# Optimization experiments

Measured on AMD Instinct MI355X. Metric: run time of the kernel, lower is better.

Reference implementation:

```python
import jax, jax.numpy as jnp
import numpy as np

D = H = W = 128
C = 16
VOXEL_SIZE = 0.05  # origin = 0, grid spans [0, 6.4]^3 in world coords
N_POINTS = 2_000_000


def setup_inputs() -> dict:
    key = jax.random.key(0)
    k1, k2 = jax.random.split(key)
    # world-space query points uniformly inside the grid bounds
    points = jax.random.uniform(k1, (N_POINTS, 3), dtype=jnp.float32) * (D * VOXEL_SIZE)
    values = jax.random.normal(k2, (D, H, W, C), dtype=jnp.float32)
    return {"points": points, "values": values}


def reference(points, values):
    # world -> grid coords (origin = 0)
    gc = points / VOXEL_SIZE  # [N, 3]
    x, y, z = gc[:, 0], gc[:, 1], gc[:, 2]

    x0 = jnp.clip(jnp.floor(x).astype(jnp.int32), 0, D - 1)
    y0 = jnp.clip(jnp.floor(y).astype(jnp.int32), 0, H - 1)
    z0 = jnp.clip(jnp.floor(z).astype(jnp.int32), 0, W - 1)
    x1 = jnp.clip(x0 + 1, 0, D - 1)
    y1 = jnp.clip(y0 + 1, 0, H - 1)
    z1 = jnp.clip(z0 + 1, 0, W - 1)

    # fractional offsets (computed against the clipped floor index, as in source)
    xd = (x - x0.astype(x.dtype))[:, None]
    yd = (y - y0.astype(y.dtype))[:, None]
    zd = (z - z0.astype(z.dtype))[:, None]

    # flatten grid for efficient single-axis gather
    flat = values.reshape(D * H * W, C)

    def gather(xi, yi, zi):
        lin = (xi * H + yi) * W + zi  # [N]
        return jnp.take(flat, lin, axis=0)  # [N, C]

    c000 = gather(x0, y0, z0)
    c001 = gather(x0, y0, z1)
    c010 = gather(x0, y1, z0)
    c011 = gather(x0, y1, z1)
    c100 = gather(x1, y0, z0)
    c101 = gather(x1, y0, z1)
    c110 = gather(x1, y1, z0)
    c111 = gather(x1, y1, z1)

    c00 = c000 * (1 - xd) + c100 * xd
    c01 = c001 * (1 - xd) + c101 * xd
    c10 = c010 * (1 - xd) + c110 * xd
    c11 = c011 * (1 - xd) + c111 * xd
    c0 = c00 * (1 - yd) + c10 * yd
    c1 = c01 * (1 - yd) + c11 * yd
    return c0 * (1 - zd) + c1 * zd  # [N, C]
```

## Files before the change

kernel.cpp:

```cpp
#include <hip/hip_runtime.h>


#define DD 128
#define HH 128
#define WW 128

__device__ __forceinline__ float4 lerp4(float4 a, float4 b, float t) {
    return make_float4(fmaf(b.x - a.x, t, a.x),
                       fmaf(b.y - a.y, t, a.y),
                       fmaf(b.z - a.z, t, a.z),
                       fmaf(b.w - a.w, t, a.w));
}

__global__ __launch_bounds__(256) void trilerp_kernel(
    const float* __restrict__ points,
    const float4* __restrict__ values,
    float4* __restrict__ out,
    int n_points)
{
    int t = blockIdx.x * blockDim.x + threadIdx.x;
    int p = t >> 2;
    int c4 = t & 3;
    if (p >= n_points) return;

    float x = points[p * 3 + 0] * 20.0f;
    float y = points[p * 3 + 1] * 20.0f;
    float z = points[p * 3 + 2] * 20.0f;

    float fx = floorf(x), fy = floorf(y), fz = floorf(z);
    int x0 = min(max((int)fx, 0), DD - 1);
    int y0 = min(max((int)fy, 0), HH - 1);
    int z0 = min(max((int)fz, 0), WW - 1);
    int x1 = min(x0 + 1, DD - 1);
    int y1 = min(y0 + 1, HH - 1);
    int z1 = min(z0 + 1, WW - 1);

    float xd = x - (float)x0;
    float yd = y - (float)y0;
    float zd = z - (float)z0;

    #define VIDX(xi, yi, zi) (((((xi) << 7) + (yi)) << 7) + (zi)) * 4 + c4

    float4 c000 = values[VIDX(x0, y0, z0)];
    float4 c001 = values[VIDX(x0, y0, z1)];
    float4 c010 = values[VIDX(x0, y1, z0)];
    float4 c011 = values[VIDX(x0, y1, z1)];
    float4 c100 = values[VIDX(x1, y0, z0)];
    float4 c101 = values[VIDX(x1, y0, z1)];
    float4 c110 = values[VIDX(x1, y1, z0)];
    float4 c111 = values[VIDX(x1, y1, z1)];
    #undef VIDX

    float4 c00 = lerp4(c000, c100, xd);
    float4 c01 = lerp4(c001, c101, xd);
    float4 c10 = lerp4(c010, c110, xd);
    float4 c11 = lerp4(c011, c111, xd);

    float4 c0 = lerp4(c00, c10, yd);
    float4 c1 = lerp4(c01, c11, yd);

    out[t] = lerp4(c0, c1, zd);
}

extern "C" void kernel_launch(void* const* d_in, const int* in_sizes, int n_in,
                              void* d_out, int out_size, void* d_ws, size_t ws_size,
                              hipStream_t stream) {
    const float* points = (const float*)d_in[0];
    const float4* values = (const float4*)d_in[1];
    float4* out = (float4*)d_out;

    int n_points = in_sizes[0] / 3;
    int total_threads = n_points * 4;
    int blocks = (total_threads + 255) / 256;

    trilerp_kernel<<<blocks, 256, 0, stream>>>(points, values, out, n_points);
}
```

Before: 414.7 us.

## Bucket-sort query points spatially before trilinear gather for cache locality

Adds a counting sort of points into 4x4x4-voxel buckets: a histogram pass, a single-block scan and an atomic scatter into a workspace buffer of (x,y,z,index). The interpolation kernel then walks the sorted points, so neighbouring threads gather nearby voxels, and writes results back by original index. This targets the random-access cost of the 128 MB value grid at the price of extra passes over the points, global atomics, scattered output writes and several more launches. A direct path is kept for when the workspace is too small.

```diff
diff --git a/kernel.cpp b/kernel.cpp
--- a/kernel.cpp
+++ b/kernel.cpp
@@ -1,9 +1,60 @@
 #include <hip/hip_runtime.h>
+#include <hip/hip_runtime_api.h>
 
 
 #define DD 128
 #define HH 128
 #define WW 128
+#define NBUCKET 32768
+
+__device__ __forceinline__ int bucket_of(float px, float py, float pz) {
+    int x0 = min(max((int)floorf(px * 20.0f), 0), DD - 1);
+    int y0 = min(max((int)floorf(py * 20.0f), 0), HH - 1);
+    int z0 = min(max((int)floorf(pz * 20.0f), 0), WW - 1);
+    return (((x0 >> 2) << 5) + (y0 >> 2)) * 32 + (z0 >> 2);
+}
+
+__global__ __launch_bounds__(256) void hist_kernel(
+    const float* __restrict__ points, unsigned int* __restrict__ hist, int n)
+{
+    int p = blockIdx.x * blockDim.x + threadIdx.x;
+    if (p >= n) return;
+    float px = points[3 * p + 0], py = points[3 * p + 1], pz = points[3 * p + 2];
+    atomicAdd(&hist[bucket_of(px, py, pz)], 1u);
+}
+
+__global__ __launch_bounds__(1024) void scan_kernel(
+    const unsigned int* __restrict__ hist, unsigned int* __restrict__ offsets)
+{
+    __shared__ unsigned int partial[1024];
+    int t = threadIdx.x;
+    unsigned int vals[32];
+    unsigned int sum = 0;
+    #pragma unroll
+    for (int i = 0; i < 32; ++i) { vals[i] = hist[t * 32 + i]; sum += vals[i]; }
+    partial[t] = sum;
+    __syncthreads();
+    for (int off = 1; off < 1024; off <<= 1) {
+        unsigned int v = (t >= off) ? partial[t - off] : 0u;
+        __syncthreads();
+        partial[t] += v;
+        __syncthreads();
+    }
+    unsigned int run = (t == 0) ? 0u : partial[t - 1];
+    #pragma unroll
+    for (int i = 0; i < 32; ++i) { offsets[t * 32 + i] = run; run += vals[i]; }
+}
+
+__global__ __launch_bounds__(256) void scatter_kernel(
+    const float* __restrict__ points, unsigned int* __restrict__ offsets,
+    float4* __restrict__ sorted, int n)
+{
+    int p = blockIdx.x * blockDim.x + threadIdx.x;
+    if (p >= n) return;
+    float px = points[3 * p + 0], py = points[3 * p + 1], pz = points[3 * p + 2];
+    unsigned int pos = atomicAdd(&offsets[bucket_of(px, py, pz)], 1u);
+    sorted[pos] = make_float4(px, py, pz, __int_as_float(p));
+}
 
 __device__ __forceinline__ float4 lerp4(float4 a, float4 b, float t) {
     return make_float4(fmaf(b.x - a.x, t, a.x),
@@ -12,8 +63,8 @@
                        fmaf(b.w - a.w, t, a.w));
 }
 
-__global__ __launch_bounds__(256) void trilerp_kernel(
-    const float* __restrict__ points,
+__global__ __launch_bounds__(256) void trilerp_sorted_kernel(
+    const float4* __restrict__ sorted,
     const float4* __restrict__ values,
     float4* __restrict__ out,
     int n_points)
@@ -23,24 +74,21 @@
     int c4 = t & 3;
     if (p >= n_points) return;
 
-    float x = points[p * 3 + 0] * 20.0f;
-    float y = points[p * 3 + 1] * 20.0f;
-    float z = points[p * 3 + 2] * 20.0f;
+    float4 s = sorted[p];
+    float x = s.x * 20.0f, y = s.y * 20.0f, z = s.z * 20.0f;
+    int idx = __float_as_int(s.w);
 
-    float fx = floorf(x), fy = floorf(y), fz = floorf(z);
-    int x0 = min(max((int)fx, 0), DD - 1);
-    int y0 = min(max((int)fy, 0), HH - 1);
-    int z0 = min(max((int)fz, 0), WW - 1);
+    int x0 = min(max((int)floorf(x), 0), DD - 1);
+    int y0 = min(max((int)floorf(y), 0), HH - 1);
+    int z0 = min(max((int)floorf(z), 0), WW - 1);
     int x1 = min(x0 + 1, DD - 1);
     int y1 = min(y0 + 1, HH - 1);
     int z1 = min(z0 + 1, WW - 1);
-
     float xd = x - (float)x0;
     float yd = y - (float)y0;
     float zd = z - (float)z0;
 
-    #define VIDX(xi, yi, zi) (((((xi) << 7) + (yi)) << 7) + (zi)) * 4 + c4
-
+    #define VIDX(xi, yi, zi) ((((((xi) << 7) + (yi)) << 7) + (zi)) * 4 + c4)
     float4 c000 = values[VIDX(x0, y0, z0)];
     float4 c001 = values[VIDX(x0, y0, z1)];
     float4 c010 = values[VIDX(x0, y1, z0)];
@@ -55,10 +103,50 @@
     float4 c01 = lerp4(c001, c101, xd);
     float4 c10 = lerp4(c010, c110, xd);
     float4 c11 = lerp4(c011, c111, xd);
-
     float4 c0 = lerp4(c00, c10, yd);
     float4 c1 = lerp4(c01, c11, yd);
+    out[idx * 4 + c4] = lerp4(c0, c1, zd);
+}
 
+__global__ __launch_bounds__(256) void trilerp_direct_kernel(
+    const float* __restrict__ points,
+    const float4* __restrict__ values,
+    float4* __restrict__ out,
+    int n_points)
+{
+    int t = blockIdx.x * blockDim.x + threadIdx.x;
+    int p = t >> 2;
+    int c4 = t & 3;
+    if (p >= n_points) return;
+
+    float x = points[p * 3 + 0] * 20.0f;
+    float y = points[p * 3 + 1] * 20.0f;
+    float z = points[p * 3 + 2] * 20.0f;
+    int x0 = min(max((int)floorf(x), 0), DD - 1);
+    int y0 = min(max((int)floorf(y), 0), HH - 1);
+    int z0 = min(max((int)floorf(z), 0), WW - 1);
+    int x1 = min(x0 + 1, DD - 1);
+    int y1 = min(y0 + 1, HH - 1);
+    int z1 = min(z0 + 1, WW - 1);
+    float xd = x - (float)x0, yd = y - (float)y0, zd = z - (float)z0;
+
+    #define VIDX(xi, yi, zi) ((((((xi) << 7) + (yi)) << 7) + (zi)) * 4 + c4)
+    float4 c000 = values[VIDX(x0, y0, z0)];
+    float4 c001 = values[VIDX(x0, y0, z1)];
+    float4 c010 = values[VIDX(x0, y1, z0)];
+    float4 c011 = values[VIDX(x0, y1, z1)];
+    float4 c100 = values[VIDX(x1, y0, z0)];
+    float4 c101 = values[VIDX(x1, y0, z1)];
+    float4 c110 = values[VIDX(x1, y1, z0)];
+    float4 c111 = values[VIDX(x1, y1, z1)];
+    #undef VIDX
+
+    float4 c00 = lerp4(c000, c100, xd);
+    float4 c01 = lerp4(c001, c101, xd);
+    float4 c10 = lerp4(c010, c110, xd);
+    float4 c11 = lerp4(c011, c111, xd);
+    float4 c0 = lerp4(c00, c10, yd);
+    float4 c1 = lerp4(c01, c11, yd);
     out[t] = lerp4(c0, c1, zd);
 }
 
@@ -70,8 +158,27 @@
     float4* out = (float4*)d_out;
 
     int n_points = in_sizes[0] / 3;
-    int total_threads = n_points * 4;
-    int blocks = (total_threads + 255) / 256;
+    size_t need = (size_t)NBUCKET * 8 + (size_t)n_points * 16;
 
-    trilerp_kernel<<<blocks, 256, 0, stream>>>(points, values, out, n_points);
+    if (ws_size < need) {
+        int total = n_points * 4;
+        trilerp_direct_kernel<<<(total + 255) / 256, 256, 0, stream>>>(
+            points, values, out, n_points);
+        return;
+    }
+
+    unsigned int* hist = (unsigned int*)d_ws;
+    unsigned int* offsets = hist + NBUCKET;
+    float4* sorted = (float4*)((char*)d_ws + (size_t)NBUCKET * 8);
+
+    hipMemsetAsync(hist, 0, NBUCKET * sizeof(unsigned int), stream);
+
+    int pblocks = (n_points + 255) / 256;
+    hist_kernel<<<pblocks, 256, 0, stream>>>(points, hist, n_points);
+    scan_kernel<<<1, 1024, 0, stream>>>(hist, offsets);
+    scatter_kernel<<<pblocks, 256, 0, stream>>>(points, offsets, sorted, n_points);
+
+    int total = n_points * 4;
+    trilerp_sorted_kernel<<<(total + 255) / 256, 256, 0, stream>>>(
+        sorted, values, out, n_points);
 }
```

Result: slower. 538.3 us (+29.8%).

## Bin query points into spatial buckets before trilinear gather for cache locality

Applied to the files above, without the earlier changes.

Adds a binning pass that atomically scatters points, tagged with their original index, into 4x4x4-voxel buckets in workspace. A per-bucket interpolation kernel then processes spatially close points together so their corner gathers share cache lines, and writes results back to each point's original position. Points that exceed the per-bucket capacity go to an overflow list handled by a third kernel. It falls back to a direct kernel when the workspace is too small. The trade is extra passes, two memsets, contended atomics and scattered output writes in exchange for far fewer random gathers from the 128 MB grid; results would be lost if overflow exceeded its fixed cap.

```diff
diff --git a/kernel.cpp b/kernel.cpp
--- a/kernel.cpp
+++ b/kernel.cpp
@@ -1,9 +1,20 @@
 #include <hip/hip_runtime.h>
+#include <hip/hip_runtime_api.h>
 
 
 #define DD 128
 #define HH 128
 #define WW 128
+#define NBUCKET 32768
+#define CNT_STRIDE 16
+#define OVF_CAP 16384
+
+__device__ __forceinline__ int bucket_of(float px, float py, float pz) {
+    int x0 = min(max((int)floorf(px * 20.0f), 0), DD - 1);
+    int y0 = min(max((int)floorf(py * 20.0f), 0), HH - 1);
+    int z0 = min(max((int)floorf(pz * 20.0f), 0), WW - 1);
+    return (((x0 >> 2) << 5) + (y0 >> 2)) * 32 + (z0 >> 2);
+}
 
 __device__ __forceinline__ float4 lerp4(float4 a, float4 b, float t) {
     return make_float4(fmaf(b.x - a.x, t, a.x),
@@ -12,35 +23,22 @@
                        fmaf(b.w - a.w, t, a.w));
 }
 
-__global__ __launch_bounds__(256) void trilerp_kernel(
-    const float* __restrict__ points,
-    const float4* __restrict__ values,
-    float4* __restrict__ out,
-    int n_points)
-{
-    int t = blockIdx.x * blockDim.x + threadIdx.x;
-    int p = t >> 2;
-    int c4 = t & 3;
-    if (p >= n_points) return;
+__device__ __forceinline__ void interp_store(float4 s, const float4* __restrict__ values,
+                                             float4* __restrict__ out, int c4) {
+    float x = s.x * 20.0f, y = s.y * 20.0f, z = s.z * 20.0f;
+    int idx = __float_as_int(s.w);
 
-    float x = points[p * 3 + 0] * 20.0f;
-    float y = points[p * 3 + 1] * 20.0f;
-    float z = points[p * 3 + 2] * 20.0f;
-
-    float fx = floorf(x), fy = floorf(y), fz = floorf(z);
-    int x0 = min(max((int)fx, 0), DD - 1);
-    int y0 = min(max((int)fy, 0), HH - 1);
-    int z0 = min(max((int)fz, 0), WW - 1);
+    int x0 = min(max((int)floorf(x), 0), DD - 1);
+    int y0 = min(max((int)floorf(y), 0), HH - 1);
+    int z0 = min(max((int)floorf(z), 0), WW - 1);
     int x1 = min(x0 + 1, DD - 1);
     int y1 = min(y0 + 1, HH - 1);
     int z1 = min(z0 + 1, WW - 1);
-
     float xd = x - (float)x0;
     float yd = y - (float)y0;
     float zd = z - (float)z0;
 
-    #define VIDX(xi, yi, zi) (((((xi) << 7) + (yi)) << 7) + (zi)) * 4 + c4
-
+    #define VIDX(xi, yi, zi) ((((((xi) << 7) + (yi)) << 7) + (zi)) * 4 + c4)
     float4 c000 = values[VIDX(x0, y0, z0)];
     float4 c001 = values[VIDX(x0, y0, z1)];
     float4 c010 = values[VIDX(x0, y1, z0)];
@@ -55,11 +53,76 @@
     float4 c01 = lerp4(c001, c101, xd);
     float4 c10 = lerp4(c010, c110, xd);
     float4 c11 = lerp4(c011, c111, xd);
-
     float4 c0 = lerp4(c00, c10, yd);
     float4 c1 = lerp4(c01, c11, yd);
+    out[idx * 4 + c4] = lerp4(c0, c1, zd);
+}
 
-    out[t] = lerp4(c0, c1, zd);
+__global__ __launch_bounds__(256) void bin_kernel(
+    const float* __restrict__ points,
+    unsigned int* __restrict__ cnt,
+    unsigned int* __restrict__ ovf_cnt,
+    float4* __restrict__ ovf,
+    float4* __restrict__ sorted,
+    int n, int cap)
+{
+    int p = blockIdx.x * blockDim.x + threadIdx.x;
+    if (p >= n) return;
+    float px = points[3 * p + 0], py = points[3 * p + 1], pz = points[3 * p + 2];
+    int b = bucket_of(px, py, pz);
+    unsigned int r = atomicAdd(&cnt[b * CNT_STRIDE], 1u);
+    float4 v = make_float4(px, py, pz, __int_as_float(p));
+    if (r < (unsigned int)cap) {
+        sorted[(size_t)b * cap + r] = v;
+    } else {
+        unsigned int o = atomicAdd(ovf_cnt, 1u);
+        if (o < OVF_CAP) ovf[o] = v;
+    }
+}
+
+__global__ __launch_bounds__(256) void trilerp_bucket_kernel(
+    const float4* __restrict__ sorted,
+    const unsigned int* __restrict__ cnt,
+    const float4* __restrict__ values,
+    float4* __restrict__ out,
+    int cap)
+{
+    int blk = blockIdx.x;
+    int b = ((blk & 7) << 12) + (blk >> 3);
+    unsigned int n = min(cnt[b * CNT_STRIDE], (unsigned int)cap);
+    int c4 = threadIdx.x & 3;
+    const float4* base = sorted + (size_t)b * cap;
+    for (unsigned int i = threadIdx.x >> 2; i < n; i += 64) {
+        interp_store(base[i], values, out, c4);
+    }
+}
+
+__global__ __launch_bounds__(256) void trilerp_ovf_kernel(
+    const float4* __restrict__ ovf,
+    const unsigned int* __restrict__ ovf_cnt,
+    const float4* __restrict__ values,
+    float4* __restrict__ out)
+{
+    unsigned int n = min(*ovf_cnt, (unsigned int)OVF_CAP);
+    int t = blockIdx.x * blockDim.x + threadIdx.x;
+    unsigned int p = (unsigned int)(t >> 2);
+    if (p >= n) return;
+    interp_store(ovf[p], values, out, t & 3);
+}
+
+__global__ __launch_bounds__(256) void trilerp_direct_kernel(
+    const float* __restrict__ points,
+    const float4* __restrict__ values,
+    float4* __restrict__ out,
+    int n_points)
+{
+    int t = blockIdx.x * blockDim.x + threadIdx.x;
+    int p = t >> 2;
+    int c4 = t & 3;
+    if (p >= n_points) return;
+    float4 s = make_float4(points[p * 3], points[p * 3 + 1], points[p * 3 + 2],
+                           __int_as_float(p));
+    interp_store(s, values, out, c4);
 }
 
 extern "C" void kernel_launch(void* const* d_in, const int* in_sizes, int n_in,
@@ -68,10 +131,32 @@
     const float* points = (const float*)d_in[0];
     const float4* values = (const float4*)d_in[1];
     float4* out = (float4*)d_out;
+    int n_points = in_sizes[0] / 3;
 
-    int n_points = in_sizes[0] / 3;
-    int total_threads = n_points * 4;
-    int blocks = (total_threads + 255) / 256;
+    size_t cnt_bytes = (size_t)NBUCKET * CNT_STRIDE * 4;
+    size_t sorted_off = cnt_bytes + (512u << 10);
+    long long avail = (long long)ws_size - (long long)sorted_off;
+    int cap = (int)(avail / ((long long)NBUCKET * 16));
+    if (cap > 96) cap = 96;
 
-    trilerp_kernel<<<blocks, 256, 0, stream>>>(points, values, out, n_points);
+    if (cap < 76) {
+        int total = n_points * 4;
+        trilerp_direct_kernel<<<(total + 255) / 256, 256, 0, stream>>>(
+            points, values, out, n_points);
+        return;
+    }
+
+    unsigned int* cnt = (unsigned int*)d_ws;
+    unsigned int* ovf_cnt = (unsigned int*)((char*)d_ws + cnt_bytes);
+    float4* ovf = (float4*)((char*)d_ws + cnt_bytes + 4096);
+    float4* sorted = (float4*)((char*)d_ws + sorted_off);
+
+    hipMemsetAsync(cnt, 0, cnt_bytes, stream);
+    hipMemsetAsync(ovf_cnt, 0, 64, stream);
+
+    int pblocks = (n_points + 255) / 256;
+    bin_kernel<<<pblocks, 256, 0, stream>>>(points, cnt, ovf_cnt, ovf, sorted,
+                                            n_points, cap);
+    trilerp_bucket_kernel<<<NBUCKET, 256, 0, stream>>>(sorted, cnt, values, out, cap);
+    trilerp_ovf_kernel<<<(OVF_CAP * 4) / 256, 256, 0, stream>>>(ovf, ovf_cnt, values, out);
 }
```

Result: slower. 453.8 us (+9.4%).
